# Kernel optimization log

Measured on AMD Instinct MI355X. Metric: run time of the kernel, lower is better.

## Reference

```python
import jax, jax.numpy as jnp
import numpy as np

NUM_HEADS = 16
DIM_IN = 1024
DIM_Q = 64
DIM_K = 64


def setup_inputs() -> dict:
    key = jax.random.key(0)
    ks = jax.random.split(key, 12)
    B, S = 4, 2048
    s_in = 1.0 / np.sqrt(DIM_IN)
    s_o = 1.0 / np.sqrt(NUM_HEADS * DIM_K)
    return {
        "Q": jax.random.normal(ks[0], (B, S, DIM_IN), jnp.float32),
        "K": jax.random.normal(ks[1], (B, S, DIM_IN), jnp.float32),
        "V": jax.random.normal(ks[2], (B, S, DIM_IN), jnp.float32),
        # per-head projection weights stacked along head axis
        "Wq": jax.random.uniform(ks[3], (NUM_HEADS, DIM_IN, DIM_Q), jnp.float32, -s_in, s_in),
        "bq": jax.random.uniform(ks[4], (NUM_HEADS, DIM_Q), jnp.float32, -s_in, s_in),
        "Wk": jax.random.uniform(ks[5], (NUM_HEADS, DIM_IN, DIM_K), jnp.float32, -s_in, s_in),
        "bk": jax.random.uniform(ks[6], (NUM_HEADS, DIM_K), jnp.float32, -s_in, s_in),
        "Wv": jax.random.uniform(ks[7], (NUM_HEADS, DIM_IN, DIM_K), jnp.float32, -s_in, s_in),
        "bv": jax.random.uniform(ks[8], (NUM_HEADS, DIM_K), jnp.float32, -s_in, s_in),
        # output projection: (num_heads*dim_k) -> dim_in
        "Wo": jax.random.uniform(ks[9], (NUM_HEADS * DIM_K, DIM_IN), jnp.float32, -s_o, s_o),
        "bo": jax.random.uniform(ks[10], (DIM_IN,), jnp.float32, -s_o, s_o),
    }


def reference(Q, K, V, Wq, bq, Wk, bk, Wv, bv, Wo, bo):
    # Batched across heads: equivalent to the per-head Python loop in the
    # original module (heads concatenated along the feature dim in order).
    q = jnp.einsum("bsd,hdq->bhsq", Q, Wq) + bq[None, :, None, :]  # [B,H,S,dq]
    k = jnp.einsum("btd,hdq->bhtq", K, Wk) + bk[None, :, None, :]  # [B,H,T,dk]
    v = jnp.einsum("btd,hdv->bhtv", V, Wv) + bv[None, :, None, :]  # [B,H,T,dv]
    scale = 1.0 / jnp.sqrt(jnp.asarray(q.shape[-1], q.dtype))
    scores = jnp.einsum("bhsq,bhtq->bhst", q, k) * scale           # [B,H,S,T]
    attn = jax.nn.softmax(scores, axis=-1)
    out = jnp.einsum("bhst,bhtv->bhsv", attn, v)                   # [B,H,S,dv]
    B, H, S, Dv = out.shape
    concat = jnp.transpose(out, (0, 2, 1, 3)).reshape(B, S, H * Dv)  # torch.cat(dim=2)
    return concat @ Wo + bo
```

## Files before the change

### kernel.cpp

```cpp
#include <hip/hip_runtime.h>

typedef short bf16x8 __attribute__((ext_vector_type(8)));
typedef float f32x4 __attribute__((ext_vector_type(4)));

#define MFMA16(a, b, c) __builtin_amdgcn_mfma_f32_16x16x32_bf16(a, b, c, 0, 0, 0)

#define SC 0.18033688011112043f

__device__ __forceinline__ unsigned short f2bf(float f) {
  union { float f; unsigned u; } v; v.f = f;
  unsigned r = v.u + 0x7FFFu + ((v.u >> 16) & 1u);
  return (unsigned short)(r >> 16);
}

__device__ __forceinline__ float exp2_fast(float x) {
  float r;
  asm("v_exp_f32 %0, %1" : "=v"(r) : "v"(x));
  return r;
}

typedef __attribute__((address_space(1))) const unsigned int gas_u32;
typedef __attribute__((address_space(3))) unsigned int las_u32;
__device__ __forceinline__ void glds16(const void* g, void* l) {
  __builtin_amdgcn_global_load_lds((gas_u32*)g, (las_u32*)l, 16, 0, 0);
}

__global__ void cvt3_kernel(const float* __restrict__ a, const float* __restrict__ b,
                            const float* __restrict__ c, unsigned short* __restrict__ da,
                            unsigned short* __restrict__ db, unsigned short* __restrict__ dc,
                            int n4) {
  const float* s = blockIdx.y == 0 ? a : (blockIdx.y == 1 ? b : c);
  unsigned short* d = blockIdx.y == 0 ? da : (blockIdx.y == 1 ? db : dc);
  int i = blockIdx.x * blockDim.x + threadIdx.x;
  int stride = gridDim.x * blockDim.x;
  for (; i < n4; i += stride) {
    float4 v = ((const float4*)s)[i];
    ushort4 o;
    o.x = f2bf(v.x); o.y = f2bf(v.y); o.z = f2bf(v.z); o.w = f2bf(v.w);
    ((ushort4*)d)[i] = o;
  }
}

template<int NSRC>
__global__ void tcvt_kernel(const float* __restrict__ s0p, const float* __restrict__ s1p,
                            const float* __restrict__ s2p, unsigned short* __restrict__ d0p,
                            unsigned short* __restrict__ d1p, unsigned short* __restrict__ d2p,
                            int R, int C) {
  __shared__ float tile[64][65];
  int z = blockIdx.z, mat = 0, zz = z;
  if (NSRC == 3) { mat = z >> 4; zz = z & 15; }
  const float* s = (mat == 0 ? s0p : (mat == 1 ? s1p : s2p)) + (size_t)zz * R * C;
  unsigned short* d = (mat == 0 ? d0p : (mat == 1 ? d1p : d2p)) + (size_t)zz * R * C;
  int r0 = blockIdx.x << 6, c0 = blockIdx.y << 6;
  int t = threadIdx.x;
  int lr = t >> 2, lc = (t & 3) << 4;
#pragma unroll
  for (int j = 0; j < 16; j += 4) {
    float4 v = *(const float4*)(s + (size_t)(r0 + lr) * C + c0 + lc + j);
    tile[lr][lc + j + 0] = v.x; tile[lr][lc + j + 1] = v.y;
    tile[lr][lc + j + 2] = v.z; tile[lr][lc + j + 3] = v.w;
  }
  __syncthreads();
  int oc = t >> 2, orr = (t & 3) << 4;
  unsigned short* dp = d + (size_t)(c0 + oc) * R + r0 + orr;
#pragma unroll
  for (int jj = 0; jj < 4; ++jj) {
    ushort4 o;
    o.x = f2bf(tile[orr + (jj << 2) + 0][oc]);
    o.y = f2bf(tile[orr + (jj << 2) + 1][oc]);
    o.z = f2bf(tile[orr + (jj << 2) + 2][oc]);
    o.w = f2bf(tile[orr + (jj << 2) + 3][oc]);
    *(ushort4*)(dp + (jj << 2)) = o;
  }
}

__global__ __launch_bounds__(256, 2)
void gemm_qkv_kernel(const unsigned short* __restrict__ Qb, const unsigned short* __restrict__ Kb,
                     const unsigned short* __restrict__ Vb,
                     const unsigned short* __restrict__ Wt,
                     const float* __restrict__ bq, const float* __restrict__ bk,
                     const float* __restrict__ bv,
                     unsigned short* __restrict__ qbuf,
                     unsigned short* __restrict__ kbuf,
                     unsigned short* __restrict__ vtbuf) {
  __shared__ unsigned short lds[16384];
  unsigned short* lds_a = lds;
  unsigned short* lds_b = lds + 8192;
  const int tid = threadIdx.x;
  const int w = tid >> 6, l = tid & 63;
  const int g = l >> 4, x = l & 15;
  const int wm = (w >> 1) << 6, wn = (w & 1) << 6;
  const int bid = blockIdx.x;
  const int xcd = bid & 7, slot = bid >> 3;
  const int sec = slot >> 6;
  const int inner = slot & 63;
  const int m0 = ((xcd << 3) + (inner >> 3)) << 7;
  const int n0 = (inner & 7) << 7;
  const int nt = (sec << 3) + (inner & 7);
  const unsigned short* A = sec == 0 ? Qb : (sec == 1 ? Kb : Vb);
  const unsigned short* W = Wt + ((size_t)nt << 17);
  const float* bias = sec == 0 ? bq : (sec == 1 ? bk : bv);
  const int lrow = l >> 3;
  const int lchk = (l & 7) ^ (lrow & 7);
  f32x4 acc[4][4] = {};
  for (int k0 = 0; k0 < 1024; k0 += 64) {
    __syncthreads();
#pragma unroll
    for (int p = 0; p < 4; ++p) {
      int rb = (w << 5) + (p << 3);
      glds16(A + ((size_t)(m0 + rb + lrow) << 10) + k0 + (lchk << 3),
             (char*)lds_a + rb * 128);
      glds16(W + ((size_t)(rb + lrow) << 10) + k0 + (lchk << 3),
             (char*)lds_b + rb * 128);
    }
    __syncthreads();
#pragma unroll
    for (int kk = 0; kk < 2; ++kk) {
      bf16x8 af[4], bfr[4];
#pragma unroll
      for (int i = 0; i < 4; ++i) {
        int m = wm + (i << 4) + x;
        af[i] = *(const bf16x8*)((const char*)lds_a + m * 128 +
                                 (((kk << 6) + (g << 4)) ^ ((m & 7) << 4)));
        int n = wn + (i << 4) + x;
        bfr[i] = *(const bf16x8*)((const char*)lds_b + n * 128 +
                                  (((kk << 6) + (g << 4)) ^ ((n & 7) << 4)));
      }
#pragma unroll
      for (int i = 0; i < 4; ++i)
#pragma unroll
        for (int j = 0; j < 4; ++j)
          acc[i][j] = MFMA16(af[i], bfr[j], acc[i][j]);
    }
  }

  if (sec < 2) {
    unsigned short* dst = sec == 0 ? qbuf : kbuf;
    const float scale = sec == 0 ? SC : 1.0f;
#pragma unroll
    for (int j = 0; j < 4; ++j) {
      int n = n0 + wn + (j << 4) + x;
      float bv2 = bias[n];
      int h = n >> 6, dd = n & 63;
#pragma unroll
      for (int i = 0; i < 4; ++i) {
#pragma unroll
        for (int r = 0; r < 4; ++r) {
          int M = m0 + wm + (i << 4) + (g << 2) + r;
          int b = M >> 11, s = M & 2047;
          dst[(size_t)(b * 16 + h) * 131072 + (size_t)s * 64 + dd] =
              f2bf((acc[i][j][r] + bv2) * scale);
        }
      }
    }
  } else {
    __syncthreads();
#pragma unroll
    for (int i = 0; i < 4; ++i)
#pragma unroll
      for (int j = 0; j < 4; ++j) {
        int nl = wn + (j << 4) + x;
        float bv2 = bias[n0 + nl];
        ushort4 pk;
        pk.x = f2bf(acc[i][j][0] + bv2);
        pk.y = f2bf(acc[i][j][1] + bv2);
        pk.z = f2bf(acc[i][j][2] + bv2);
        pk.w = f2bf(acc[i][j][3] + bv2);
        int ml = wm + (i << 4) + (g << 2);
        *(ushort4*)((char*)lds + nl * 256 + ((ml * 2) ^ ((nl & 7) << 4))) = pk;
      }
    __syncthreads();
    int nl = tid >> 1, half = tid & 1;
    int n = n0 + nl, h = n >> 6, dd = n & 63;
    int bb = m0 >> 11;
    size_t base = ((size_t)(bb * 16 + h) * 64 + dd) * 2048 + (m0 & 2047) + (half << 6);
#pragma unroll
    for (int c = 0; c < 8; ++c) {
      int mb = (half << 7) + (c << 4);
      uint4 vv = *(const uint4*)((char*)lds + nl * 256 + (mb ^ ((nl & 7) << 4)));
      *(uint4*)(vtbuf + base + (c << 3)) = vv;
    }
  }
}

__global__ __launch_bounds__(256, 2)
void gemm_o_kernel(const unsigned short* __restrict__ A,
                   const unsigned short* __restrict__ W,
                   const float* __restrict__ bias,
                   float* __restrict__ dst) {
  __shared__ unsigned short lds[16384];
  unsigned short* lds_a = lds;
  unsigned short* lds_b = lds + 8192;
  const int tid = threadIdx.x;
  const int w = tid >> 6, l = tid & 63;
  const int g = l >> 4, x = l & 15;
  const int wm = (w >> 1) << 6, wn = (w & 1) << 6;
  const int bid = blockIdx.x;
  const int xcd = bid & 7, slot = bid >> 3;
  const int m0 = ((xcd << 3) + (slot & 7)) << 7;
  const int n0 = (slot >> 3) << 7;
  const int lrow = l >> 3;
  const int lchk = (l & 7) ^ (lrow & 7);
  f32x4 acc[4][4] = {};
  for (int k0 = 0; k0 < 1024; k0 += 64) {
    __syncthreads();
#pragma unroll
    for (int p = 0; p < 4; ++p) {
      int rb = (w << 5) + (p << 3);
      glds16(A + ((size_t)(m0 + rb + lrow) << 10) + k0 + (lchk << 3),
             (char*)lds_a + rb * 128);
      glds16(W + ((size_t)(n0 + rb + lrow) << 10) + k0 + (lchk << 3),
             (char*)lds_b + rb * 128);
    }
    __syncthreads();
#pragma unroll
    for (int kk = 0; kk < 2; ++kk) {
      bf16x8 af[4], bfr[4];
#pragma unroll
      for (int i = 0; i < 4; ++i) {
        int m = wm + (i << 4) + x;
        af[i] = *(const bf16x8*)((const char*)lds_a + m * 128 +
                                 (((kk << 6) + (g << 4)) ^ ((m & 7) << 4)));
        int n = wn + (i << 4) + x;
        bfr[i] = *(const bf16x8*)((const char*)lds_b + n * 128 +
                                  (((kk << 6) + (g << 4)) ^ ((n & 7) << 4)));
      }
#pragma unroll
      for (int i = 0; i < 4; ++i)
#pragma unroll
        for (int j = 0; j < 4; ++j)
          acc[i][j] = MFMA16(af[i], bfr[j], acc[i][j]);
    }
  }
#pragma unroll
  for (int j = 0; j < 4; ++j) {
    int n = n0 + wn + (j << 4) + x;
    float bv = bias[n];
#pragma unroll
    for (int i = 0; i < 4; ++i) {
#pragma unroll
      for (int r = 0; r < 4; ++r) {
        int M = m0 + wm + (i << 4) + (g << 2) + r;
        dst[(size_t)M * 1024 + n] = acc[i][j][r] + bv;
      }
    }
  }
}

__device__ __forceinline__ void softmax_pack(const f32x4* s, bf16x8& o0, bf16x8& o1) {
  unsigned pk[4][2];
#pragma unroll
  for (int tt = 0; tt < 4; ++tt) {
    float p0 = exp2_fast(s[tt][0]);
    float p1 = exp2_fast(s[tt][1]);
    float p2 = exp2_fast(s[tt][2]);
    float p3 = exp2_fast(s[tt][3]);
    asm("v_cvt_pk_bf16_f32 %0, %1, %2" : "=v"(pk[tt][0]) : "v"(p0), "v"(p1));
    asm("v_cvt_pk_bf16_f32 %0, %1, %2" : "=v"(pk[tt][1]) : "v"(p2), "v"(p3));
  }
  union { unsigned u[4]; bf16x8 v; } w0, w1;
#pragma unroll
  for (int p = 0; p < 2; ++p) {
    unsigned X = pk[0][p], Y = pk[1][p];
    asm("v_permlane32_swap_b32 %0, %1" : "+v"(X), "+v"(Y));
    asm("v_permlane16_swap_b32 %0, %1" : "+v"(X), "+v"(Y));
    w0.u[p] = X; w0.u[2 + p] = Y;
    unsigned X2 = pk[2][p], Y2 = pk[3][p];
    asm("v_permlane32_swap_b32 %0, %1" : "+v"(X2), "+v"(Y2));
    asm("v_permlane16_swap_b32 %0, %1" : "+v"(X2), "+v"(Y2));
    w1.u[p] = X2; w1.u[2 + p] = Y2;
  }
  o0 = w0.v; o1 = w1.v;
}

__global__ __attribute__((amdgpu_flat_work_group_size(512, 512), amdgpu_waves_per_eu(4, 8)))
void flash_kernel(const unsigned short* __restrict__ qb,
                  const unsigned short* __restrict__ kb,
                  const unsigned short* __restrict__ vtb,
                  unsigned short* __restrict__ out) {
  __shared__ unsigned short lds_k[2][4096];
  __shared__ unsigned short lds_v[2][4096];
  const int tid = threadIdx.x, w = tid >> 6, l = tid & 63;
  const int g = l >> 4, x = l & 15;
  const int bid = blockIdx.x;
  const int xcd = bid & 7, slot = bid >> 3;
  const int bh = (xcd << 3) + (slot >> 3);
  const int s0 = (slot & 7) << 8;
  const size_t boff = (size_t)bh << 17;
  const int str = tid >> 3, stc = (tid & 7) << 3;
  const int swb = str * 128 + ((stc << 1) ^ ((str & 7) << 4));
  const unsigned short* ksrc = kb + boff + ((size_t)str << 6) + stc;
  const unsigned short* vsrc = vtb + boff + ((size_t)str << 11) + stc;
  const bf16x8 ones = {(short)0x3F80, (short)0x3F80, (short)0x3F80, (short)0x3F80,
                       (short)0x3F80, (short)0x3F80, (short)0x3F80, (short)0x3F80};
  bf16x8 qf0[2], qf1[2];
#pragma unroll
  for (int i = 0; i < 2; ++i) {
    const unsigned short* qp = qb + boff + ((size_t)(s0 + (w << 5) + (i << 4) + x) << 6);
    qf0[i] = *(const bf16x8*)(qp + (g << 3));
    qf1[i] = *(const bf16x8*)(qp + 32 + (g << 3));
  }
  f32x4 accA[4] = {}, accB[4] = {};
  f32x4 accSA = {}, accSB = {};
  {
    uint4 kv = *(const uint4*)ksrc;
    uint4 vv = *(const uint4*)vsrc;
    *(uint4*)((char*)lds_k[0] + swb) = kv;
    *(uint4*)((char*)lds_v[0] + swb) = vv;
  }
  __syncthreads();
  int cur = 0;
  for (int t0 = 0; t0 < 2048; t0 += 64) {
    const bool more = t0 < 1984;
    uint4 nk, nv;
    if (more) {
      nk = *(const uint4*)(ksrc + ((size_t)(t0 + 64) << 6));
      nv = *(const uint4*)(vsrc + t0 + 64);
    }
    f32x4 sA[4], sB[4];
#pragma unroll
    for (int tt = 0; tt < 4; ++tt) {
      int trow = (tt << 4) + x;
      const char* kr = (const char*)lds_k[cur] + trow * 128;
      int sw = (trow & 7) << 4;
      bf16x8 k0 = *(const bf16x8*)(kr + ((g << 4) ^ sw));
      bf16x8 k1 = *(const bf16x8*)(kr + ((64 + (g << 4)) ^ sw));
      __builtin_amdgcn_s_setprio(1);
      f32x4 t4 = {};
      t4 = MFMA16(k0, qf0[0], t4);
      t4 = MFMA16(k1, qf1[0], t4);
      sA[tt] = t4;
      f32x4 u4 = {};
      u4 = MFMA16(k0, qf0[1], u4);
      u4 = MFMA16(k1, qf1[1], u4);
      sB[tt] = u4;
      __builtin_amdgcn_s_setprio(0);
    }
    bf16x8 paA[2], paB[2];
    softmax_pack(sA, paA[0], paA[1]);
    softmax_pack(sB, paB[0], paB[1]);
    __builtin_amdgcn_s_setprio(1);
    accSA = MFMA16(paA[0], ones, accSA);
    accSA = MFMA16(paA[1], ones, accSA);
    accSB = MFMA16(paB[0], ones, accSB);
    accSB = MFMA16(paB[1], ones, accSB);
    __builtin_amdgcn_s_setprio(0);
#pragma unroll
    for (int kk = 0; kk < 2; ++kk) {
#pragma unroll
      for (int nn = 0; nn < 4; ++nn) {
        int dv = (nn << 4) + x;
        bf16x8 vb = *(const bf16x8*)((const char*)lds_v[cur] + dv * 128 +
                                     (((kk << 6) + (g << 4)) ^ ((dv & 7) << 4)));
        __builtin_amdgcn_s_setprio(1);
        accA[nn] = MFMA16(paA[kk], vb, accA[nn]);
        accB[nn] = MFMA16(paB[kk], vb, accB[nn]);
        __builtin_amdgcn_s_setprio(0);
      }
    }
    if (more) {
      int nb = cur ^ 1;
      *(uint4*)((char*)lds_k[nb] + swb) = nk;
      *(uint4*)((char*)lds_v[nb] + swb) = nv;
    }
    __syncthreads();
    cur ^= 1;
  }
  const int b = bh >> 4, h = bh & 15;
#pragma unroll
  for (int i = 0; i < 2; ++i) {
    f32x4& as = i == 0 ? accSA : accSB;
    f32x4* ac = i == 0 ? accA : accB;
    float iv[4];
#pragma unroll
    for (int r = 0; r < 4; ++r) iv[r] = 1.f / as[r];
    const int srow = s0 + (w << 5) + (i << 4) + (g << 2);
#pragma unroll
    for (int nn = 0; nn < 4; ++nn) {
      int dv = (nn << 4) + x;
      size_t base = ((size_t)(b * 2048 + srow)) * 1024 + (h << 6) + dv;
      out[base]        = f2bf(ac[nn][0] * iv[0]);
      out[base + 1024] = f2bf(ac[nn][1] * iv[1]);
      out[base + 2048] = f2bf(ac[nn][2] * iv[2]);
      out[base + 3072] = f2bf(ac[nn][3] * iv[3]);
    }
  }
}

extern "C" void kernel_launch(void* const* d_in, const int* in_sizes, int n_in,
                              void* d_out, int out_size, void* d_ws, size_t ws_size,
                              hipStream_t stream) {
  const float* Q  = (const float*)d_in[0];
  const float* K  = (const float*)d_in[1];
  const float* V  = (const float*)d_in[2];
  const float* Wq = (const float*)d_in[3];
  const float* bq = (const float*)d_in[4];
  const float* Wk = (const float*)d_in[5];
  const float* bk = (const float*)d_in[6];
  const float* Wv = (const float*)d_in[7];
  const float* bv = (const float*)d_in[8];
  const float* Wo = (const float*)d_in[9];
  const float* bo = (const float*)d_in[10];

  if (ws_size < 109051904u) return;

  char* ws = (char*)d_ws;
  unsigned short* Qb    = (unsigned short*)(ws + 0);
  unsigned short* Kb    = (unsigned short*)(ws + 16777216);
  unsigned short* Vb    = (unsigned short*)(ws + 33554432);
  unsigned short* Wtq   = (unsigned short*)(ws + 50331648);
  unsigned short* Wtk   = (unsigned short*)(ws + 52428800);
  unsigned short* Wtv   = (unsigned short*)(ws + 54525952);
  unsigned short* Wot   = (unsigned short*)(ws + 56623104);
  unsigned short* qbuf  = (unsigned short*)(ws + 58720256);
  unsigned short* kbuf  = (unsigned short*)(ws + 75497472);
  unsigned short* vtbuf = (unsigned short*)(ws + 92274688);
  unsigned short* concat = Qb;

  cvt3_kernel<<<dim3(1024, 3), 256, 0, stream>>>(Q, K, V, Qb, Kb, Vb, 2097152);
  tcvt_kernel<3><<<dim3(16, 1, 48), 256, 0, stream>>>(Wq, Wk, Wv, Wtq, Wtk, Wtv, 1024, 64);
  tcvt_kernel<1><<<dim3(16, 16, 1), 256, 0, stream>>>(Wo, Wo, Wo, Wot, Wot, Wot, 1024, 1024);
  gemm_qkv_kernel<<<1536, 256, 0, stream>>>(Qb, Kb, Vb, Wtq, bq, bk, bv, qbuf, kbuf, vtbuf);
  flash_kernel<<<512, 512, 0, stream>>>(qbuf, kbuf, vtbuf, concat);
  gemm_o_kernel<<<512, 256, 0, stream>>>(concat, Wot, bo, (float*)d_out);
}
```

Before: 200.3 us.

## Fuse fp32-to-bf16 activation conversion into QKV GEMM tile loads

Removes the standalone cvt3 kernel that converted Q, K and V to bf16 in workspace. The QKV GEMM now streams fp32 activations straight into LDS through a swizzled layout and converts them to bf16 in registers with v_cvt_pk_bf16_f32 before the MFMA. This avoids writing and re-reading 48 MB of bf16 intermediates and one launch. In exchange the GEMM reads twice the bytes per A tile, since each tile is now re-read in fp32 by the 8 N-tiles. LDS grows to 48 KB per block, which may limit occupancy.

```diff
diff --git a/kernel.cpp b/kernel.cpp
--- a/kernel.cpp
+++ b/kernel.cpp
@@ -23,22 +23,6 @@
 typedef __attribute__((address_space(3))) unsigned int las_u32;
 __device__ __forceinline__ void glds16(const void* g, void* l) {
   __builtin_amdgcn_global_load_lds((gas_u32*)g, (las_u32*)l, 16, 0, 0);
-}
-
-__global__ void cvt3_kernel(const float* __restrict__ a, const float* __restrict__ b,
-                            const float* __restrict__ c, unsigned short* __restrict__ da,
-                            unsigned short* __restrict__ db, unsigned short* __restrict__ dc,
-                            int n4) {
-  const float* s = blockIdx.y == 0 ? a : (blockIdx.y == 1 ? b : c);
-  unsigned short* d = blockIdx.y == 0 ? da : (blockIdx.y == 1 ? db : dc);
-  int i = blockIdx.x * blockDim.x + threadIdx.x;
-  int stride = gridDim.x * blockDim.x;
-  for (; i < n4; i += stride) {
-    float4 v = ((const float4*)s)[i];
-    ushort4 o;
-    o.x = f2bf(v.x); o.y = f2bf(v.y); o.z = f2bf(v.z); o.w = f2bf(v.w);
-    ((ushort4*)d)[i] = o;
-  }
 }
 
 template<int NSRC>
@@ -75,17 +59,17 @@
 }
 
 __global__ __launch_bounds__(256, 2)
-void gemm_qkv_kernel(const unsigned short* __restrict__ Qb, const unsigned short* __restrict__ Kb,
-                     const unsigned short* __restrict__ Vb,
+void gemm_qkv_kernel(const float* __restrict__ Qf, const float* __restrict__ Kf,
+                     const float* __restrict__ Vf,
                      const unsigned short* __restrict__ Wt,
                      const float* __restrict__ bq, const float* __restrict__ bk,
                      const float* __restrict__ bv,
                      unsigned short* __restrict__ qbuf,
                      unsigned short* __restrict__ kbuf,
                      unsigned short* __restrict__ vtbuf) {
-  __shared__ unsigned short lds[16384];
-  unsigned short* lds_a = lds;
-  unsigned short* lds_b = lds + 8192;
+  __shared__ __align__(16) char ldsc[49152];
+  float* lds_a32 = (float*)ldsc;
+  unsigned short* lds_b = (unsigned short*)(ldsc + 32768);
   const int tid = threadIdx.x;
   const int w = tid >> 6, l = tid & 63;
   const int g = l >> 4, x = l & 15;
@@ -97,19 +81,29 @@
   const int m0 = ((xcd << 3) + (inner >> 3)) << 7;
   const int n0 = (inner & 7) << 7;
   const int nt = (sec << 3) + (inner & 7);
-  const unsigned short* A = sec == 0 ? Qb : (sec == 1 ? Kb : Vb);
+  const float* A = sec == 0 ? Qf : (sec == 1 ? Kf : Vf);
   const unsigned short* W = Wt + ((size_t)nt << 17);
   const float* bias = sec == 0 ? bq : (sec == 1 ? bk : bv);
   const int lrow = l >> 3;
   const int lchk = (l & 7) ^ (lrow & 7);
+  const int rl4 = l >> 4;
+  const int c32 = (l & 15) >> 1;
+  const int h16 = l & 1;
+  const int offA0 = (((c32 ^ rl4) << 3) + (h16 << 2));
+  const float* baseA0 = A + ((size_t)(m0 + rl4) << 10) + offA0;
+  const float* baseA1 = A + ((size_t)(m0 + rl4) << 10) + (offA0 ^ 32);
   f32x4 acc[4][4] = {};
   for (int k0 = 0; k0 < 1024; k0 += 64) {
     __syncthreads();
 #pragma unroll
+    for (int p = 0; p < 8; ++p) {
+      int rb = (w << 5) + (p << 2);
+      const float* src = ((p & 1) ? baseA1 : baseA0) + ((size_t)rb << 10) + k0;
+      glds16(src, (char*)lds_a32 + rb * 256);
+    }
+#pragma unroll
     for (int p = 0; p < 4; ++p) {
       int rb = (w << 5) + (p << 3);
-      glds16(A + ((size_t)(m0 + rb + lrow) << 10) + k0 + (lchk << 3),
-             (char*)lds_a + rb * 128);
       glds16(W + ((size_t)(rb + lrow) << 10) + k0 + (lchk << 3),
              (char*)lds_b + rb * 128);
     }
@@ -120,8 +114,16 @@
 #pragma unroll
       for (int i = 0; i < 4; ++i) {
         int m = wm + (i << 4) + x;
-        af[i] = *(const bf16x8*)((const char*)lds_a + m * 128 +
-                                 (((kk << 6) + (g << 4)) ^ ((m & 7) << 4)));
+        const char* ar = (const char*)lds_a32 + m * 256;
+        int ba = ((kk << 7) | (g << 5)) ^ ((m & 7) << 5);
+        f32x4 lo = *(const f32x4*)(ar + ba);
+        f32x4 hi = *(const f32x4*)(ar + ba + 16);
+        union { unsigned u[4]; bf16x8 v; } cu;
+        asm("v_cvt_pk_bf16_f32 %0, %1, %2" : "=v"(cu.u[0]) : "v"(lo[0]), "v"(lo[1]));
+        asm("v_cvt_pk_bf16_f32 %0, %1, %2" : "=v"(cu.u[1]) : "v"(lo[2]), "v"(lo[3]));
+        asm("v_cvt_pk_bf16_f32 %0, %1, %2" : "=v"(cu.u[2]) : "v"(hi[0]), "v"(hi[1]));
+        asm("v_cvt_pk_bf16_f32 %0, %1, %2" : "=v"(cu.u[3]) : "v"(hi[2]), "v"(hi[3]));
+        af[i] = cu.v;
         int n = wn + (i << 4) + x;
         bfr[i] = *(const bf16x8*)((const char*)lds_b + n * 128 +
                                   (((kk << 6) + (g << 4)) ^ ((n & 7) << 4)));
@@ -167,7 +169,7 @@
         pk.z = f2bf(acc[i][j][2] + bv2);
         pk.w = f2bf(acc[i][j][3] + bv2);
         int ml = wm + (i << 4) + (g << 2);
-        *(ushort4*)((char*)lds + nl * 256 + ((ml * 2) ^ ((nl & 7) << 4))) = pk;
+        *(ushort4*)(ldsc + nl * 256 + ((ml * 2) ^ ((nl & 7) << 4))) = pk;
       }
     __syncthreads();
     int nl = tid >> 1, half = tid & 1;
@@ -177,7 +179,7 @@
 #pragma unroll
     for (int c = 0; c < 8; ++c) {
       int mb = (half << 7) + (c << 4);
-      uint4 vv = *(const uint4*)((char*)lds + nl * 256 + (mb ^ ((nl & 7) << 4)));
+      uint4 vv = *(const uint4*)(ldsc + nl * 256 + (mb ^ ((nl & 7) << 4)));
       *(uint4*)(vtbuf + base + (c << 3)) = vv;
     }
   }
@@ -405,9 +407,7 @@
   if (ws_size < 109051904u) return;
 
   char* ws = (char*)d_ws;
-  unsigned short* Qb    = (unsigned short*)(ws + 0);
-  unsigned short* Kb    = (unsigned short*)(ws + 16777216);
-  unsigned short* Vb    = (unsigned short*)(ws + 33554432);
+  unsigned short* concat = (unsigned short*)(ws + 0);
   unsigned short* Wtq   = (unsigned short*)(ws + 50331648);
   unsigned short* Wtk   = (unsigned short*)(ws + 52428800);
   unsigned short* Wtv   = (unsigned short*)(ws + 54525952);
@@ -415,12 +415,10 @@
   unsigned short* qbuf  = (unsigned short*)(ws + 58720256);
   unsigned short* kbuf  = (unsigned short*)(ws + 75497472);
   unsigned short* vtbuf = (unsigned short*)(ws + 92274688);
-  unsigned short* concat = Qb;
-
-  cvt3_kernel<<<dim3(1024, 3), 256, 0, stream>>>(Q, K, V, Qb, Kb, Vb, 2097152);
+
   tcvt_kernel<3><<<dim3(16, 1, 48), 256, 0, stream>>>(Wq, Wk, Wv, Wtq, Wtk, Wtv, 1024, 64);
   tcvt_kernel<1><<<dim3(16, 16, 1), 256, 0, stream>>>(Wo, Wo, Wo, Wot, Wot, Wot, 1024, 1024);
-  gemm_qkv_kernel<<<1536, 256, 0, stream>>>(Qb, Kb, Vb, Wtq, bq, bk, bv, qbuf, kbuf, vtbuf);
+  gemm_qkv_kernel<<<1536, 256, 0, stream>>>(Q, K, V, Wtq, bq, bk, bv, qbuf, kbuf, vtbuf);
   flash_kernel<<<512, 512, 0, stream>>>(qbuf, kbuf, vtbuf, concat);
   gemm_o_kernel<<<512, 256, 0, stream>>>(concat, Wot, bo, (float*)d_out);
 }
```

Result: faster. 183.5 us (median of 4 runs) (-8.4%).
